# Kernel optimization log

Hardware: AMD Instinct MI355X
Metric: run time of the kernel (lower is better)

## Reference

```python
import jax, jax.numpy as jnp
import numpy as np


def setup_inputs() -> dict:
    key = jax.random.key(0)
    ks = jax.random.split(key, 8)
    N, D_in = 4096, 1024
    H1, H2, H3 = 2048, 2048, 1024
    D_out = 512

    def init_w(k, fan_in, shape):
        return jax.random.normal(k, shape, dtype=jnp.float32) / jnp.sqrt(jnp.float32(fan_in))

    return {
        "features": jax.random.normal(ks[0], (N, D_in), dtype=jnp.float32),
        "W1": init_w(ks[1], D_in, (D_in, H1)),
        "b1": jnp.zeros((H1,), dtype=jnp.float32),
        "W2": init_w(ks[2], H1, (H1, H2)),
        "b2": jnp.zeros((H2,), dtype=jnp.float32),
        "W3": init_w(ks[3], H2, (H2, H3)),
        "b3": jnp.zeros((H3,), dtype=jnp.float32),
        "Wh": init_w(ks[4], H3, (H3, D_out)),
        "bh": jnp.zeros((D_out,), dtype=jnp.float32),
        "w": init_w(ks[5], D_out, (D_out, N)),
    }


def reference(features, W1, b1, W2, b2, W3, b3, Wh, bh, w):
    # MLP backbone (torchvision MLP: ReLU after each hidden layer except last)
    h = jax.nn.relu(features @ W1 + b1)          # [N, H1]
    h = jax.nn.relu(h @ W2 + b2)                 # [N, H2]
    h = h @ W3 + b3                              # [N, H3] (no activation on last)
    logits = h @ Wh + bh                         # [N, D_out]
    # diag(logits @ w) computed as row-wise dot product -> [N]
    out = jnp.einsum("nk,kn->n", logits, w)
    return out
```

## Files before the change

kernel.cpp:

```cpp
#include <hip/hip_runtime.h>
#include <cstdint>
#include <cstddef>

typedef unsigned short u16;
typedef __attribute__((ext_vector_type(8))) short bf16x8;
typedef __attribute__((ext_vector_type(8))) unsigned short u16x8;
typedef __attribute__((ext_vector_type(4))) unsigned short u16x4;
typedef __attribute__((ext_vector_type(4))) float f32x4;

__device__ __forceinline__ u16 f2b(float f) {
    union { float f; uint32_t u; } v; v.f = f;
    uint32_t u = v.u;
    uint32_t r = (u + 0x7FFFu + ((u >> 16) & 1u)) >> 16;
    return (u16)r;
}
__device__ __forceinline__ float b2f(u16 b) {
    union { uint32_t u; float f; } v; v.u = ((uint32_t)b) << 16;
    return v.f;
}
__device__ __forceinline__ void gload_lds16(const void* g, void* l) {
    __builtin_amdgcn_global_load_lds(
        (const __attribute__((address_space(1))) void*)g,
        (__attribute__((address_space(3))) void*)l,
        16, 0, 0);
}

__device__ __forceinline__ void cvt_fat(const float* __restrict__ in,
                                        u16* __restrict__ outp, int bb, int tid) {
#pragma unroll
    for (int it = 0; it < 8; ++it) {
        size_t u = (size_t)bb * 2048 + (size_t)it * 256 + tid;
        size_t base = u * 8;
        const float4* p = (const float4*)(in + base);
        float4 a = p[0], c = p[1];
        u16x8 o;
        o[0] = f2b(a.x); o[1] = f2b(a.y); o[2] = f2b(a.z); o[3] = f2b(a.w);
        o[4] = f2b(c.x); o[5] = f2b(c.y); o[6] = f2b(c.z); o[7] = f2b(c.w);
        *(u16x8*)(outp + base) = o;
    }
}

__device__ __forceinline__ void transpose64_256(const float* __restrict__ in,
                                                u16* __restrict__ outp,
                                                int K, int N, int t, int tid,
                                                float (*tile)[65]) {
    const int ntx = N >> 6;
    const int n0 = (t % ntx) * 64, k0 = (t / ntx) * 64;
    const int r0 = tid >> 4, c4 = tid & 15;
#pragma unroll
    for (int j = 0; j < 4; ++j) {
        int r = r0 + j * 16;
        float4 v = *(const float4*)(in + (size_t)(k0 + r) * N + n0 + c4 * 4);
        tile[r][c4 * 4 + 0] = v.x; tile[r][c4 * 4 + 1] = v.y;
        tile[r][c4 * 4 + 2] = v.z; tile[r][c4 * 4 + 3] = v.w;
    }
    __syncthreads();
    const int rr = tid >> 2;
#pragma unroll
    for (int j = 0; j < 4; ++j) {
        int ch = (tid & 3) + j * 4;
        u16x4 o;
        o[0] = f2b(tile[ch * 4 + 0][rr]); o[1] = f2b(tile[ch * 4 + 1][rr]);
        o[2] = f2b(tile[ch * 4 + 2][rr]); o[3] = f2b(tile[ch * 4 + 3][rr]);
        *(u16x4*)(outp + (size_t)(n0 + rr) * K + k0 + ch * 4) = o;
    }
    __syncthreads();
}

__device__ __forceinline__ void transpose64_512(const float* __restrict__ in,
                                                u16* __restrict__ outp,
                                                int K, int N, int t, int tid,
                                                float (*tile)[65]) {
    const int ntx = N >> 6;
    const int n0 = (t % ntx) * 64, k0 = (t / ntx) * 64;
    const int r0 = tid >> 4, c4 = tid & 15;
#pragma unroll
    for (int j = 0; j < 2; ++j) {
        int r = r0 + j * 32;
        float4 v = *(const float4*)(in + (size_t)(k0 + r) * N + n0 + c4 * 4);
        tile[r][c4 * 4 + 0] = v.x; tile[r][c4 * 4 + 1] = v.y;
        tile[r][c4 * 4 + 2] = v.z; tile[r][c4 * 4 + 3] = v.w;
    }
    __syncthreads();
    const int rr = tid >> 3;
#pragma unroll
    for (int j = 0; j < 2; ++j) {
        int ch = (tid & 7) + j * 8;
        u16x4 o;
        o[0] = f2b(tile[ch * 4 + 0][rr]); o[1] = f2b(tile[ch * 4 + 1][rr]);
        o[2] = f2b(tile[ch * 4 + 2][rr]); o[3] = f2b(tile[ch * 4 + 3][rr]);
        *(u16x4*)(outp + (size_t)(n0 + rr) * K + k0 + ch * 4) = o;
    }
    __syncthreads();
}

__global__ __launch_bounds__(256) void prep1_kernel(
    const float* __restrict__ feat, u16* __restrict__ featB,
    const float* __restrict__ W1, u16* __restrict__ W1T,
    const float* __restrict__ W3, u16* __restrict__ W3c,
    const float* __restrict__ Wh, u16* __restrict__ WhT,
    const float* __restrict__ b3, const float* __restrict__ bh,
    float* __restrict__ b34) {
    __shared__ float tile[64][65];
    const int b = blockIdx.x, tid = threadIdx.x;
    if (b < 256) { cvt_fat(feat, featB, b, tid); return; }
    if (b < 384) { cvt_fat(W3, W3c, b - 256, tid); return; }
    if (b < 512) {
        int g = b - 384;
#pragma unroll
        for (int j = 0; j < 4; ++j)
            transpose64_256(W1, W1T, 1024, 2048, g * 4 + j, tid, tile);
        return;
    }
    if (b < 544) {
        int g = b - 512;
#pragma unroll
        for (int j = 0; j < 4; ++j)
            transpose64_256(Wh, WhT, 1024, 512, g * 4 + j, tid, tile);
        return;
    }
    {
        int g = b - 544;
        int jl = tid & 15, kg = tid >> 4;
        int j = g * 16 + jl;
        float s = 0.f;
#pragma unroll 8
        for (int kk = 0; kk < 64; ++kk) {
            int k = kg * 64 + kk;
            s += b3[k] * Wh[(size_t)k * 512 + j];
        }
        tile[kg][jl] = s;
        __syncthreads();
        if (kg == 0) {
            float t = bh[j];
#pragma unroll
            for (int q = 0; q < 16; ++q) t += tile[q][jl];
            b34[j] = t;
        }
    }
}


__device__ __forceinline__ void stage_q(const u16* __restrict__ g, int ldg,
                                        u16* lds, int tid) {
    int r = tid >> 3;
    int ch = (tid & 7) ^ (r & 7);
    gload_lds16(g + (size_t)r * ldg + ch * 8, (char*)lds + tid * 16);
}

__device__ __forceinline__ bf16x8 lds_frag(const u16* s, int row, int kk, int lg) {
    int byte = (row << 7) + (kk << 6) + (lg << 4);
    byte ^= (row & 7) << 4;
    return *(const bf16x8*)((const char*)s + byte);
}

#define MFMA_CLUSTER(AF, BF)                                                   \
    do {                                                                       \
        __builtin_amdgcn_s_setprio(1);                                         \
        _Pragma("unroll") for (int m = 0; m < 4; ++m)                          \
            _Pragma("unroll") for (int n = 0; n < 4; ++n)                      \
                acc[m][n] = __builtin_amdgcn_mfma_f32_16x16x32_bf16(           \
                    AF[m], BF[n], acc[m][n], 0, 0, 0);                         \
        __builtin_amdgcn_s_setprio(0);                                         \
    } while (0)

__device__ __forceinline__ void gemm_loop(
    const u16* __restrict__ Ag, const u16* __restrict__ Bg, int K,
    u16* sA, u16* sB, f32x4 (&acc)[4][4],
    int tid, int wm, int wn, int lr, int lg) {
    const int nt = K >> 6;
    stage_q(Ag, K, sA, tid);
    stage_q(Ag + (size_t)64 * K, K, sA + 4096, tid);
    stage_q(Ag + (size_t)128 * K, K, sA + 8192, tid);
    stage_q(Ag + (size_t)192 * K, K, sA + 12288, tid);
    stage_q(Bg, K, sB, tid);
    stage_q(Bg + (size_t)64 * K, K, sB + 4096, tid);
    stage_q(Ag + 64, K, sA + 16384, tid);
    stage_q(Ag + (size_t)64 * K + 64, K, sA + 16384 + 4096, tid);
    stage_q(Ag + (size_t)128 * K + 64, K, sA + 16384 + 8192, tid);
    stage_q(Ag + (size_t)192 * K + 64, K, sA + 16384 + 12288, tid);
    stage_q(Bg + 64, K, sB + 8192, tid);
    stage_q(Bg + (size_t)64 * K + 64, K, sB + 8192 + 4096, tid);
    asm volatile("s_waitcnt vmcnt(6)" ::: "memory");
    __builtin_amdgcn_sched_barrier(0);
    __builtin_amdgcn_s_barrier();

    for (int t = 0; t < nt; ++t) {
        const int cb = t % 3, nb = (t + 2) % 3;
        const u16* sAc = sA + cb * 16384;
        const u16* sBc = sB + cb * 8192;
        u16* sAn = sA + nb * 16384;
        u16* sBn = sB + nb * 8192;
        const int kb = (t + 2) << 6;
        const bool more2 = (t + 2) < nt;

        bf16x8 a0[4], b0[4];
#pragma unroll
        for (int m = 0; m < 4; ++m)
            a0[m] = lds_frag(sAc + wm * 4096, m * 16 + lr, 0, lg);
#pragma unroll
        for (int n = 0; n < 4; ++n)
            b0[n] = lds_frag(sBc + wn * 4096, n * 16 + lr, 0, lg);
        if (more2) {
            stage_q(Bg + kb, K, sBn, tid);
            stage_q(Bg + (size_t)64 * K + kb, K, sBn + 4096, tid);
            stage_q(Ag + kb, K, sAn, tid);
        }
        asm volatile("s_waitcnt lgkmcnt(0)" ::: "memory");
        __builtin_amdgcn_sched_barrier(0);
        MFMA_CLUSTER(a0, b0);
        __builtin_amdgcn_s_barrier();

        bf16x8 a1[4], b1[4];
#pragma unroll
        for (int m = 0; m < 4; ++m)
            a1[m] = lds_frag(sAc + wm * 4096, m * 16 + lr, 1, lg);
#pragma unroll
        for (int n = 0; n < 4; ++n)
            b1[n] = lds_frag(sBc + wn * 4096, n * 16 + lr, 1, lg);
        if (more2) {
            stage_q(Ag + (size_t)64 * K + kb, K, sAn + 4096, tid);
            stage_q(Ag + (size_t)128 * K + kb, K, sAn + 8192, tid);
            stage_q(Ag + (size_t)192 * K + kb, K, sAn + 12288, tid);
            asm volatile("s_waitcnt vmcnt(6)" ::: "memory");
        } else if (t + 1 < nt) {
            asm volatile("s_waitcnt vmcnt(0)" ::: "memory");
        }
        __builtin_amdgcn_sched_barrier(0);
        asm volatile("s_waitcnt lgkmcnt(0)" ::: "memory");
        __builtin_amdgcn_sched_barrier(0);
        MFMA_CLUSTER(a1, b1);
        __builtin_amdgcn_s_barrier();
    }
}

template <int RELU, int HB>
__device__ __forceinline__ void gemm_store(
    const u16* __restrict__ A, const u16* __restrict__ BT,
    const float* __restrict__ bias, u16* __restrict__ C,
    int N, int K, int bx, int by, u16* sA, u16* sB) {
    const int tid = threadIdx.x;
    const int lane = tid & 63;
    const int wv = tid >> 6;
    const int wm = wv >> 1, wn = wv & 1;
    const int lr = lane & 15, lg = lane >> 4;
    const int rowBase = by * 256, colBase = bx * 128;
    f32x4 acc[4][4] = {};
    gemm_loop(A + (size_t)rowBase * K, BT + (size_t)colBase * K, K,
              sA, sB, acc, tid, wm, wn, lr, lg);
#pragma unroll
    for (int n = 0; n < 4; ++n) {
        int col = colBase + wn * 64 + n * 16 + lr;
        float bv = HB ? bias[col] : 0.f;
#pragma unroll
        for (int m = 0; m < 4; ++m) {
            int row0 = rowBase + wm * 64 + m * 16 + lg * 4;
#pragma unroll
            for (int i = 0; i < 4; ++i) {
                float v = acc[m][n][i] + bv;
                if (RELU) v = v > 0.f ? v : 0.f;
                C[(size_t)(row0 + i) * N + col] = f2b(v);
            }
        }
    }
}

__global__ __launch_bounds__(512, 2) void midA_kernel(
    const u16* __restrict__ featB, const u16* __restrict__ W1T,
    const float* __restrict__ b1, u16* __restrict__ h1,
    const u16* __restrict__ W3c, const u16* __restrict__ WhT, u16* __restrict__ W34,
    const float* __restrict__ b34, const float* __restrict__ w,
    float* __restrict__ out,
    const float* __restrict__ W2, u16* __restrict__ W2T,
    u16* __restrict__ wTb) {
    __shared__ __align__(16) u16 sA[3 * 16384];
    __shared__ __align__(16) u16 sB[3 * 8192];
    const int b = blockIdx.x, tid = threadIdx.x;
    if (b < 256) {
        gemm_store<1, 1>(featB, W1T, b1, h1, 2048, 1024, b & 15, b >> 4, sA, sB);
    } else if (b < 288) {
        int g = b - 256;
        gemm_store<0, 0>(W3c, WhT, nullptr, W34, 512, 1024, g & 3, g >> 2, sA, sB);
    } else if (b < 352) {
        int g = b - 288;
        int nl = tid & 63, jg = tid >> 6;
        int n = g * 64 + nl;
        float s = 0.f;
#pragma unroll 8
        for (int jj = 0; jj < 64; ++jj) {
            int j = jg * 64 + jj;
            s += b34[j] * w[(size_t)j * 4096 + n];
        }
        float* red = (float*)sA;
        red[jg * 64 + nl] = s;
        __syncthreads();
        if (jg == 0) {
            float t = 0.f;
#pragma unroll
            for (int q = 0; q < 8; ++q) t += red[q * 64 + nl];
            out[n] = t;
        }
    } else if (b < 1376) {
        transpose64_512(W2, W2T, 2048, 2048, b - 352, tid, (float(*)[65])sA);
    } else {
        transpose64_512(w, wTb, 512, 4096, b - 1376, tid, (float(*)[65])sA);
    }
}

__global__ __launch_bounds__(512, 2) void gemm2dot_kernel(
    const u16* __restrict__ h1, const u16* __restrict__ W2T,
    const float* __restrict__ b2,
    const u16* __restrict__ wTb, const u16* __restrict__ W34,
    float* __restrict__ out) {
    __shared__ __align__(16) u16 sA[3 * 16384];
    __shared__ __align__(16) u16 sB[3 * 8192];
    const int tid = threadIdx.x;
    const int lane = tid & 63;
    const int wv = tid >> 6;
    const int wm = wv >> 1, wn = wv & 1;
    const int lr = lane & 15, lg = lane >> 4;
    const int by = blockIdx.x >> 4, bx = blockIdx.x & 15;
    const int rowBase = by * 256, colBase = bx * 128;

    f32x4 acc[4][4] = {};
    gemm_loop(wTb + (size_t)rowBase * 512, W34 + (size_t)colBase * 512, 512,
              sA, sB, acc, tid, wm, wn, lr, lg);
    u16x4 ut16[4][4];
#pragma unroll
    for (int m = 0; m < 4; ++m)
#pragma unroll
        for (int n = 0; n < 4; ++n) {
#pragma unroll
            for (int i = 0; i < 4; ++i) ut16[m][n][i] = f2b(acc[m][n][i]);
            acc[m][n] = (f32x4){0.f, 0.f, 0.f, 0.f};
        }
    gemm_loop(h1 + (size_t)rowBase * 2048, W2T + (size_t)colBase * 2048, 2048,
              sA, sB, acc, tid, wm, wn, lr, lg);
    float psum[4][4] = {};
#pragma unroll
    for (int n = 0; n < 4; ++n) {
        int col = colBase + wn * 64 + n * 16 + lr;
        float bv = b2[col];
#pragma unroll
        for (int m = 0; m < 4; ++m)
#pragma unroll
            for (int i = 0; i < 4; ++i) {
                float v = acc[m][n][i] + bv;
                v = v > 0.f ? v : 0.f;
                psum[m][i] += v * b2f(ut16[m][n][i]);
            }
    }
#pragma unroll
    for (int m = 0; m < 4; ++m)
#pragma unroll
        for (int i = 0; i < 4; ++i) {
#pragma unroll
            for (int mask = 1; mask < 16; mask <<= 1)
                psum[m][i] += __shfl_xor(psum[m][i], mask);
        }
    if (lr == 0) {
#pragma unroll
        for (int m = 0; m < 4; ++m) {
            int row0 = rowBase + wm * 64 + m * 16 + lg * 4;
#pragma unroll
            for (int i = 0; i < 4; ++i)
                atomicAdd(&out[row0 + i], psum[m][i]);
        }
    }
}

extern "C" void kernel_launch(void* const* d_in, const int* in_sizes, int n_in,
                              void* d_out, int out_size, void* d_ws, size_t ws_size,
                              hipStream_t stream) {
    const float* features = (const float*)d_in[0];
    const float* W1 = (const float*)d_in[1];
    const float* b1 = (const float*)d_in[2];
    const float* W2 = (const float*)d_in[3];
    const float* b2 = (const float*)d_in[4];
    const float* W3 = (const float*)d_in[5];
    const float* b3 = (const float*)d_in[6];
    const float* Wh = (const float*)d_in[7];
    const float* bh = (const float*)d_in[8];
    const float* w  = (const float*)d_in[9];
    float* out = (float*)d_out;

    size_t off = 0;
    auto alloc = [&](size_t bytes) {
        void* p = (char*)d_ws + off;
        off += (bytes + 255) & ~(size_t)255;
        return p;
    };
    u16* featB = (u16*)alloc((size_t)4096 * 1024 * 2);
    u16* W3c   = (u16*)alloc((size_t)2048 * 1024 * 2);
    u16* W1T   = (u16*)alloc((size_t)2048 * 1024 * 2);
    u16* WhT   = (u16*)alloc((size_t)512 * 1024 * 2);
    u16* W2T   = (u16*)alloc((size_t)2048 * 2048 * 2);
    u16* wTb   = (u16*)alloc((size_t)4096 * 512 * 2);
    u16* W34   = (u16*)alloc((size_t)2048 * 512 * 2);
    float* b34 = (float*)alloc((size_t)512 * 4);
    u16* h1    = (u16*)alloc((size_t)4096 * 2048 * 2);

    prep1_kernel<<<576, 256, 0, stream>>>(features, featB, W1, W1T,
                                          W3, W3c, Wh, WhT, b3, bh, b34);

    midA_kernel<<<1888, 512, 0, stream>>>(featB, W1T, b1, h1,
                                          W3c, WhT, W34, b34, w, out,
                                          W2, W2T, wTb);

    gemm2dot_kernel<<<256, 512, 0, stream>>>(h1, W2T, b2, wTb, W34, out);
}
```

Before: 101.0 us.

## Split W3·Wh product over K into two fp32 partials, summed in consumer

The W3×Wh fused weight GEMM is split into two K-halves run by twice as many blocks, each writing an fp32 partial. The second kernel then sums the two partials and converts to bf16 while staging its B tile, replacing the pipelined gemm_loop for that first GEMM with a simple non-pipelined loop. The aim is to shorten the critical path of the small W34 GEMM inside midA. The cost is extra fp32 traffic and an unpipelined staging loop in gemm2dot.

Result: no change. 101.5 us (+0.5%).

```diff
diff --git a/kernel.cpp b/kernel.cpp
--- a/kernel.cpp
+++ b/kernel.cpp
@@ -165,22 +165,22 @@
     } while (0)
 
 __device__ __forceinline__ void gemm_loop(
-    const u16* __restrict__ Ag, const u16* __restrict__ Bg, int K,
+    const u16* __restrict__ Ag, const u16* __restrict__ Bg, int ld, int Klen,
     u16* sA, u16* sB, f32x4 (&acc)[4][4],
     int tid, int wm, int wn, int lr, int lg) {
-    const int nt = K >> 6;
-    stage_q(Ag, K, sA, tid);
-    stage_q(Ag + (size_t)64 * K, K, sA + 4096, tid);
-    stage_q(Ag + (size_t)128 * K, K, sA + 8192, tid);
-    stage_q(Ag + (size_t)192 * K, K, sA + 12288, tid);
-    stage_q(Bg, K, sB, tid);
-    stage_q(Bg + (size_t)64 * K, K, sB + 4096, tid);
-    stage_q(Ag + 64, K, sA + 16384, tid);
-    stage_q(Ag + (size_t)64 * K + 64, K, sA + 16384 + 4096, tid);
-    stage_q(Ag + (size_t)128 * K + 64, K, sA + 16384 + 8192, tid);
-    stage_q(Ag + (size_t)192 * K + 64, K, sA + 16384 + 12288, tid);
-    stage_q(Bg + 64, K, sB + 8192, tid);
-    stage_q(Bg + (size_t)64 * K + 64, K, sB + 8192 + 4096, tid);
+    const int nt = Klen >> 6;
+    stage_q(Ag, ld, sA, tid);
+    stage_q(Ag + (size_t)64 * ld, ld, sA + 4096, tid);
+    stage_q(Ag + (size_t)128 * ld, ld, sA + 8192, tid);
+    stage_q(Ag + (size_t)192 * ld, ld, sA + 12288, tid);
+    stage_q(Bg, ld, sB, tid);
+    stage_q(Bg + (size_t)64 * ld, ld, sB + 4096, tid);
+    stage_q(Ag + 64, ld, sA + 16384, tid);
+    stage_q(Ag + (size_t)64 * ld + 64, ld, sA + 16384 + 4096, tid);
+    stage_q(Ag + (size_t)128 * ld + 64, ld, sA + 16384 + 8192, tid);
+    stage_q(Ag + (size_t)192 * ld + 64, ld, sA + 16384 + 12288, tid);
+    stage_q(Bg + 64, ld, sB + 8192, tid);
+    stage_q(Bg + (size_t)64 * ld + 64, ld, sB + 8192 + 4096, tid);
     asm volatile("s_waitcnt vmcnt(6)" ::: "memory");
     __builtin_amdgcn_sched_barrier(0);
     __builtin_amdgcn_s_barrier();
@@ -202,9 +202,9 @@
         for (int n = 0; n < 4; ++n)
             b0[n] = lds_frag(sBc + wn * 4096, n * 16 + lr, 0, lg);
         if (more2) {
-            stage_q(Bg + kb, K, sBn, tid);
-            stage_q(Bg + (size_t)64 * K + kb, K, sBn + 4096, tid);
-            stage_q(Ag + kb, K, sAn, tid);
+            stage_q(Bg + kb, ld, sBn, tid);
+            stage_q(Bg + (size_t)64 * ld + kb, ld, sBn + 4096, tid);
+            stage_q(Ag + kb, ld, sAn, tid);
         }
         asm volatile("s_waitcnt lgkmcnt(0)" ::: "memory");
         __builtin_amdgcn_sched_barrier(0);
@@ -219,9 +219,9 @@
         for (int n = 0; n < 4; ++n)
             b1[n] = lds_frag(sBc + wn * 4096, n * 16 + lr, 1, lg);
         if (more2) {
-            stage_q(Ag + (size_t)64 * K + kb, K, sAn + 4096, tid);
-            stage_q(Ag + (size_t)128 * K + kb, K, sAn + 8192, tid);
-            stage_q(Ag + (size_t)192 * K + kb, K, sAn + 12288, tid);
+            stage_q(Ag + (size_t)64 * ld + kb, ld, sAn + 4096, tid);
+            stage_q(Ag + (size_t)128 * ld + kb, ld, sAn + 8192, tid);
+            stage_q(Ag + (size_t)192 * ld + kb, ld, sAn + 12288, tid);
             asm volatile("s_waitcnt vmcnt(6)" ::: "memory");
         } else if (t + 1 < nt) {
             asm volatile("s_waitcnt vmcnt(0)" ::: "memory");
@@ -238,7 +238,7 @@
 __device__ __forceinline__ void gemm_store(
     const u16* __restrict__ A, const u16* __restrict__ BT,
     const float* __restrict__ bias, u16* __restrict__ C,
-    int N, int K, int bx, int by, u16* sA, u16* sB) {
+    int N, int ld, int Klen, int bx, int by, u16* sA, u16* sB) {
     const int tid = threadIdx.x;
     const int lane = tid & 63;
     const int wv = tid >> 6;
@@ -246,7 +246,7 @@
     const int lr = lane & 15, lg = lane >> 4;
     const int rowBase = by * 256, colBase = bx * 128;
     f32x4 acc[4][4] = {};
-    gemm_loop(A + (size_t)rowBase * K, BT + (size_t)colBase * K, K,
+    gemm_loop(A + (size_t)rowBase * ld, BT + (size_t)colBase * ld, ld, Klen,
               sA, sB, acc, tid, wm, wn, lr, lg);
 #pragma unroll
     for (int n = 0; n < 4; ++n) {
@@ -265,10 +265,36 @@
     }
 }
 
+__device__ __forceinline__ void gemm_store_f32(
+    const u16* __restrict__ A, const u16* __restrict__ BT, float* __restrict__ C,
+    int N, int ld, int Klen, int bx, int by, u16* sA, u16* sB) {
+    const int tid = threadIdx.x;
+    const int lane = tid & 63;
+    const int wv = tid >> 6;
+    const int wm = wv >> 1, wn = wv & 1;
+    const int lr = lane & 15, lg = lane >> 4;
+    const int rowBase = by * 256, colBase = bx * 128;
+    f32x4 acc[4][4] = {};
+    gemm_loop(A + (size_t)rowBase * ld, BT + (size_t)colBase * ld, ld, Klen,
+              sA, sB, acc, tid, wm, wn, lr, lg);
+#pragma unroll
+    for (int n = 0; n < 4; ++n) {
+        int col = colBase + wn * 64 + n * 16 + lr;
+#pragma unroll
+        for (int m = 0; m < 4; ++m) {
+            int row0 = rowBase + wm * 64 + m * 16 + lg * 4;
+#pragma unroll
+            for (int i = 0; i < 4; ++i)
+                C[(size_t)(row0 + i) * N + col] = acc[m][n][i];
+        }
+    }
+}
+
 __global__ __launch_bounds__(512, 2) void midA_kernel(
     const u16* __restrict__ featB, const u16* __restrict__ W1T,
     const float* __restrict__ b1, u16* __restrict__ h1,
-    const u16* __restrict__ W3c, const u16* __restrict__ WhT, u16* __restrict__ W34,
+    const u16* __restrict__ W3c, const u16* __restrict__ WhT,
+    float* __restrict__ W34f0, float* __restrict__ W34f1,
     const float* __restrict__ b34, const float* __restrict__ w,
     float* __restrict__ out,
     const float* __restrict__ W2, u16* __restrict__ W2T,
@@ -277,12 +303,16 @@
     __shared__ __align__(16) u16 sB[3 * 8192];
     const int b = blockIdx.x, tid = threadIdx.x;
     if (b < 256) {
-        gemm_store<1, 1>(featB, W1T, b1, h1, 2048, 1024, b & 15, b >> 4, sA, sB);
-    } else if (b < 288) {
+        gemm_store<1, 1>(featB, W1T, b1, h1, 2048, 1024, 1024,
+                         b & 15, b >> 4, sA, sB);
+    } else if (b < 320) {
         int g = b - 256;
-        gemm_store<0, 0>(W3c, WhT, nullptr, W34, 512, 1024, g & 3, g >> 2, sA, sB);
-    } else if (b < 352) {
-        int g = b - 288;
+        int kh = g >> 5, gg = g & 31;
+        gemm_store_f32(W3c + kh * 512, WhT + kh * 512,
+                       kh ? W34f1 : W34f0,
+                       512, 1024, 512, gg & 3, gg >> 2, sA, sB);
+    } else if (b < 384) {
+        int g = b - 320;
         int nl = tid & 63, jg = tid >> 6;
         int n = g * 64 + nl;
         float s = 0.f;
@@ -300,17 +330,18 @@
             for (int q = 0; q < 8; ++q) t += red[q * 64 + nl];
             out[n] = t;
         }
-    } else if (b < 1376) {
-        transpose64_512(W2, W2T, 2048, 2048, b - 352, tid, (float(*)[65])sA);
+    } else if (b < 1408) {
+        transpose64_512(W2, W2T, 2048, 2048, b - 384, tid, (float(*)[65])sA);
     } else {
-        transpose64_512(w, wTb, 512, 4096, b - 1376, tid, (float(*)[65])sA);
+        transpose64_512(w, wTb, 512, 4096, b - 1408, tid, (float(*)[65])sA);
     }
 }
 
 __global__ __launch_bounds__(512, 2) void gemm2dot_kernel(
     const u16* __restrict__ h1, const u16* __restrict__ W2T,
     const float* __restrict__ b2,
-    const u16* __restrict__ wTb, const u16* __restrict__ W34,
+    const u16* __restrict__ wTb,
+    const float* __restrict__ W34f0, const float* __restrict__ W34f1,
     float* __restrict__ out) {
     __shared__ __align__(16) u16 sA[3 * 16384];
     __shared__ __align__(16) u16 sB[3 * 8192];
@@ -323,8 +354,54 @@
     const int rowBase = by * 256, colBase = bx * 128;
 
     f32x4 acc[4][4] = {};
-    gemm_loop(wTb + (size_t)rowBase * 512, W34 + (size_t)colBase * 512, 512,
-              sA, sB, acc, tid, wm, wn, lr, lg);
+
+    {
+        const u16* Ag = wTb + (size_t)rowBase * 512;
+        const float* B0 = W34f0 + (size_t)colBase * 512;
+        const float* B1 = W34f1 + (size_t)colBase * 512;
+        for (int t = 0; t < 8; ++t) {
+            const int kb = t << 6;
+            __builtin_amdgcn_s_barrier();
+            stage_q(Ag + kb, 512, sA, tid);
+            stage_q(Ag + (size_t)64 * 512 + kb, 512, sA + 4096, tid);
+            stage_q(Ag + (size_t)128 * 512 + kb, 512, sA + 8192, tid);
+            stage_q(Ag + (size_t)192 * 512 + kb, 512, sA + 12288, tid);
+#pragma unroll
+            for (int q = 0; q < 2; ++q) {
+                int cc = tid + q * 512;
+                int r = cc >> 3;
+                int ch = (cc & 7) ^ (r & 7);
+                const float4* p0 = (const float4*)(B0 + (size_t)r * 512 + kb + ch * 8);
+                const float4* p1 = (const float4*)(B1 + (size_t)r * 512 + kb + ch * 8);
+                float4 x0 = p0[0], x1 = p0[1];
+                float4 y0 = p1[0], y1 = p1[1];
+                u16x8 o;
+                o[0] = f2b(x0.x + y0.x); o[1] = f2b(x0.y + y0.y);
+                o[2] = f2b(x0.z + y0.z); o[3] = f2b(x0.w + y0.w);
+                o[4] = f2b(x1.x + y1.x); o[5] = f2b(x1.y + y1.y);
+                o[6] = f2b(x1.z + y1.z); o[7] = f2b(x1.w + y1.w);
+                *(u16x8*)((char*)sB + cc * 16) = o;
+            }
+            asm volatile("s_waitcnt vmcnt(0) lgkmcnt(0)" ::: "memory");
+            __builtin_amdgcn_sched_barrier(0);
+            __builtin_amdgcn_s_barrier();
+            bf16x8 a0[4], b0[4], a1[4], b1[4];
+#pragma unroll
+            for (int m = 0; m < 4; ++m) {
+                a0[m] = lds_frag(sA + wm * 4096, m * 16 + lr, 0, lg);
+                a1[m] = lds_frag(sA + wm * 4096, m * 16 + lr, 1, lg);
+            }
+#pragma unroll
+            for (int n = 0; n < 4; ++n) {
+                b0[n] = lds_frag(sB + wn * 4096, n * 16 + lr, 0, lg);
+                b1[n] = lds_frag(sB + wn * 4096, n * 16 + lr, 1, lg);
+            }
+            MFMA_CLUSTER(a0, b0);
+            MFMA_CLUSTER(a1, b1);
+        }
+        __builtin_amdgcn_s_barrier();
+    }
+
     u16x4 ut16[4][4];
 #pragma unroll
     for (int m = 0; m < 4; ++m)
@@ -334,8 +411,10 @@
             for (int i = 0; i < 4; ++i) ut16[m][n][i] = f2b(acc[m][n][i]);
             acc[m][n] = (f32x4){0.f, 0.f, 0.f, 0.f};
         }
-    gemm_loop(h1 + (size_t)rowBase * 2048, W2T + (size_t)colBase * 2048, 2048,
-              sA, sB, acc, tid, wm, wn, lr, lg);
+
+    gemm_loop(h1 + (size_t)rowBase * 2048, W2T + (size_t)colBase * 2048,
+              2048, 2048, sA, sB, acc, tid, wm, wn, lr, lg);
+
     float psum[4][4] = {};
 #pragma unroll
     for (int n = 0; n < 4; ++n) {
@@ -390,22 +469,24 @@
         off += (bytes + 255) & ~(size_t)255;
         return p;
     };
-    u16* featB = (u16*)alloc((size_t)4096 * 1024 * 2);
-    u16* W3c   = (u16*)alloc((size_t)2048 * 1024 * 2);
-    u16* W1T   = (u16*)alloc((size_t)2048 * 1024 * 2);
-    u16* WhT   = (u16*)alloc((size_t)512 * 1024 * 2);
-    u16* W2T   = (u16*)alloc((size_t)2048 * 2048 * 2);
-    u16* wTb   = (u16*)alloc((size_t)4096 * 512 * 2);
-    u16* W34   = (u16*)alloc((size_t)2048 * 512 * 2);
-    float* b34 = (float*)alloc((size_t)512 * 4);
-    u16* h1    = (u16*)alloc((size_t)4096 * 2048 * 2);
+    u16* featB  = (u16*)alloc((size_t)4096 * 1024 * 2);
+    u16* W3c    = (u16*)alloc((size_t)2048 * 1024 * 2);
+    u16* W1T    = (u16*)alloc((size_t)2048 * 1024 * 2);
+    u16* WhT    = (u16*)alloc((size_t)512 * 1024 * 2);
+    u16* W2T    = (u16*)alloc((size_t)2048 * 2048 * 2);
+    u16* wTb    = (u16*)alloc((size_t)4096 * 512 * 2);
+    float* W34f0 = (float*)alloc((size_t)2048 * 512 * 4);
+    float* W34f1 = (float*)alloc((size_t)2048 * 512 * 4);
+    float* b34  = (float*)alloc((size_t)512 * 4);
+    u16* h1     = (u16*)alloc((size_t)4096 * 2048 * 2);
 
     prep1_kernel<<<576, 256, 0, stream>>>(features, featB, W1, W1T,
                                           W3, W3c, Wh, WhT, b3, bh, b34);
 
-    midA_kernel<<<1888, 512, 0, stream>>>(featB, W1T, b1, h1,
-                                          W3c, WhT, W34, b34, w, out,
-                                          W2, W2T, wTb);
-
-    gemm2dot_kernel<<<256, 512, 0, stream>>>(h1, W2T, b2, wTb, W34, out);
-}
+    midA_kernel<<<1920, 512, 0, stream>>>(featB, W1T, b1, h1,
+                                          W3c, WhT, W34f0, W34f1,
+                                          b34, w, out, W2, W2T, wTb);
+
+    gemm2dot_kernel<<<256, 512, 0, stream>>>(h1, W2T, b2, wTb,
+                                             W34f0, W34f1, out);
+}
```
